# Kernel optimization log

Hardware: AMD Instinct MI355X
Metric: run time of the kernel (lower is better)

Reference implementation:

```python
import jax, jax.numpy as jnp
import numpy as np

N = 3072
E = 32 * N
H = 8
IN_F = 64
OUT_F = 16
ALPHA = 0.2  # LeakyReLU slope
NEG_INF = -9e15


def setup_inputs() -> dict:
    key = jax.random.key(0)
    k1, k2, k3, k4, k5 = jax.random.split(key, 5)
    h = jax.random.normal(k1, (N, IN_F), dtype=jnp.float32)
    edge_index = jax.random.randint(k2, (2, E), 0, N, dtype=jnp.int64)
    S = jax.random.uniform(k3, (N, N), dtype=jnp.float32)
    W = jax.random.normal(k4, (H, IN_F, OUT_F), dtype=jnp.float32) * 0.2
    a = jax.random.normal(k5, (H, 2 * OUT_F, 1), dtype=jnp.float32) * 0.3
    raw_gamma = jnp.ones((H,), dtype=jnp.float32)
    return {"h": h, "edge_index": edge_index, "S": S, "W": W, "a": a, "raw_gamma": raw_gamma}


def reference(h, edge_index, S, W, a, raw_gamma):
    n = h.shape[0]
    # dense adjacency from edge list (to_dense_adj semantics: adj[src, dst] += 1)
    adj = jnp.zeros((n, n), dtype=h.dtype).at[edge_index[0], edge_index[1]].add(1.0)
    # per-head projection: Wh [H, N, O]
    Wh = jnp.einsum('nf,hfo->hno', h, W)
    o = W.shape[2]
    a1 = a[:, :o, 0]  # [H, O]
    a2 = a[:, o:, 0]  # [H, O]
    e1 = jnp.einsum('hno,ho->hn', Wh, a1)  # Wh @ a[:O]
    e2 = jnp.einsum('hno,ho->hn', Wh, a2)  # Wh @ a[O:]
    e = jax.nn.leaky_relu(e1[:, :, None] + e2[:, None, :], ALPHA)  # [H, N, N]
    att = jnp.where(adj[None] > 0, e, jnp.asarray(NEG_INF, e.dtype))
    gamma = jax.nn.softplus(raw_gamma)  # [H], non-negative gate
    att = att * (1.0 + gamma[:, None, None] * S[None])
    att = jax.nn.softmax(att, axis=-1)  # row softmax (dim=1 of [N, N])
    # dropout is identity in eval mode
    h_prime = jnp.einsum('hnm,hmo->hno', att, Wh)  # [H, N, O]
    h_prime = jax.nn.elu(h_prime)  # concat=True per head
    # concat heads along feature dim -> [N, H*O]
    return jnp.transpose(h_prime, (1, 0, 2)).reshape(n, -1)
```

## Files before the change

kernel.cpp:

```cpp
#include <hip/hip_runtime.h>
#include <math.h>

#define N_NODES 3072
#define H_HEADS 8
#define IN_FEAT 64
#define OUT_FEAT 16
#define WORDS_PER_ROW (N_NODES / 32)
#define MAXD 1024

__global__ void zero_bits_kernel(unsigned int* __restrict__ bits, int n) {
    int i = blockIdx.x * blockDim.x + threadIdx.x;
    if (i < n) bits[i] = 0u;
}

__global__ void scatter_edges_kernel(const int* __restrict__ ei,
                                     unsigned int* __restrict__ bits, int E) {
    int e = blockIdx.x * blockDim.x + threadIdx.x;
    if (e >= E) return;
    int r = ei[e];
    int c = ei[E + e];
    atomicOr(&bits[r * WORDS_PER_ROW + (c >> 5)], 1u << (c & 31));
}

__global__ void compute_wh_kernel(const float* __restrict__ hfeat,
                                  const float* __restrict__ W,
                                  const float* __restrict__ a,
                                  float* __restrict__ Wh,
                                  float* __restrict__ e1,
                                  float* __restrict__ e2) {
    __shared__ float sh[IN_FEAT];
    int n = blockIdx.x;
    int tid = threadIdx.x;
    if (tid < IN_FEAT) sh[tid] = hfeat[n * IN_FEAT + tid];
    __syncthreads();
    int hh = tid >> 4, o = tid & 15;
    const float* wp = &W[hh * IN_FEAT * OUT_FEAT + o];
    float acc = 0.f;
#pragma unroll
    for (int f = 0; f < IN_FEAT; ++f) acc = fmaf(sh[f], wp[f * OUT_FEAT], acc);
    Wh[(hh * N_NODES + n) * OUT_FEAT + o] = acc;
    float p1 = acc * a[hh * 2 * OUT_FEAT + o];
    float p2 = acc * a[hh * 2 * OUT_FEAT + OUT_FEAT + o];
#pragma unroll
    for (int m = 1; m < 16; m <<= 1) {
        p1 += __shfl_xor(p1, m, 64);
        p2 += __shfl_xor(p2, m, 64);
    }
    if (o == 0) {
        e1[hh * N_NODES + n] = p1;
        e2[hh * N_NODES + n] = p2;
    }
}

__launch_bounds__(512)
__global__ void gat_main_kernel(const unsigned int* __restrict__ bits,
                                const float* __restrict__ S,
                                const float* __restrict__ Wh,
                                const float* __restrict__ e1,
                                const float* __restrict__ e2,
                                const float* __restrict__ raw_gamma,
                                float* __restrict__ out) {
    __shared__ int lds_j[MAXD];
    __shared__ float lds_s[MAXD];
    __shared__ int cnt_sh;
    __shared__ int fb_j;
    int i = blockIdx.x;
    int tid = threadIdx.x;
    if (tid == 0) cnt_sh = 0;
    __syncthreads();

    for (int w = tid; w < WORDS_PER_ROW; w += blockDim.x) {
        unsigned int b = bits[i * WORDS_PER_ROW + w];
        while (b) {
            int bit = __ffs(b) - 1;
            b &= b - 1;
            int j = w * 32 + bit;
            int pos = atomicAdd(&cnt_sh, 1);
            if (pos < MAXD) {
                lds_j[pos] = j;
                lds_s[pos] = S[i * N_NODES + j];
            }
        }
    }
    __syncthreads();
    int cnt = cnt_sh;
    if (cnt > MAXD) cnt = MAXD;

    int wave = tid >> 6, lane = tid & 63;
    int hh = wave;

    if (cnt == 0) {
        if (tid < 64) {
            float bm = 3.4e38f;
            int bj = 0;
            for (int j = tid; j < N_NODES; j += 64) {
                float s = S[i * N_NODES + j];
                if (s < bm) { bm = s; bj = j; }
            }
            for (int m = 1; m < 64; m <<= 1) {
                float bm2 = __shfl_xor(bm, m, 64);
                int bj2 = __shfl_xor(bj, m, 64);
                if (bm2 < bm || (bm2 == bm && bj2 < bj)) { bm = bm2; bj = bj2; }
            }
            if (tid == 0) fb_j = bj;
        }
        __syncthreads();
        int jj = fb_j;
        if (lane < OUT_FEAT) {
            float x = Wh[(hh * N_NODES + jj) * OUT_FEAT + lane];
            out[i * (H_HEADS * OUT_FEAT) + hh * OUT_FEAT + lane] =
                x > 0.f ? x : expm1f(x);
        }
        return;
    }

    float g = log1pf(expf(raw_gamma[hh]));
    float e1v = e1[hh * N_NODES + i];
    float m = -3.4e38f, l = 0.f;
    float acc[OUT_FEAT];
#pragma unroll
    for (int o = 0; o < OUT_FEAT; ++o) acc[o] = 0.f;

    for (int k = lane; k < cnt; k += 64) {
        int j = lds_j[k];
        float x = e1v + e2[hh * N_NODES + j];
        x = x > 0.f ? x : 0.2f * x;
        float v = x * (1.f + g * lds_s[k]);
        float mn = fmaxf(m, v);
        float sc = __expf(m - mn);
        float p = __expf(v - mn);
        l = l * sc + p;
        const float4* whp = (const float4*)&Wh[(hh * N_NODES + j) * OUT_FEAT];
        float4 w0 = whp[0], w1 = whp[1], w2 = whp[2], w3 = whp[3];
        acc[0] = acc[0] * sc + p * w0.x;  acc[1] = acc[1] * sc + p * w0.y;
        acc[2] = acc[2] * sc + p * w0.z;  acc[3] = acc[3] * sc + p * w0.w;
        acc[4] = acc[4] * sc + p * w1.x;  acc[5] = acc[5] * sc + p * w1.y;
        acc[6] = acc[6] * sc + p * w1.z;  acc[7] = acc[7] * sc + p * w1.w;
        acc[8] = acc[8] * sc + p * w2.x;  acc[9] = acc[9] * sc + p * w2.y;
        acc[10] = acc[10] * sc + p * w2.z; acc[11] = acc[11] * sc + p * w2.w;
        acc[12] = acc[12] * sc + p * w3.x; acc[13] = acc[13] * sc + p * w3.y;
        acc[14] = acc[14] * sc + p * w3.z; acc[15] = acc[15] * sc + p * w3.w;
        m = mn;
    }

    for (int msk = 1; msk < 64; msk <<= 1) {
        float m2 = __shfl_xor(m, msk, 64);
        float l2 = __shfl_xor(l, msk, 64);
        float mn = fmaxf(m, m2);
        float s1 = __expf(m - mn);
        float s2 = __expf(m2 - mn);
        l = l * s1 + l2 * s2;
#pragma unroll
        for (int o = 0; o < OUT_FEAT; ++o) {
            float av = __shfl_xor(acc[o], msk, 64);
            acc[o] = acc[o] * s1 + av * s2;
        }
        m = mn;
    }

    float inv = 1.f / l;
    float val = 0.f;
#pragma unroll
    for (int o = 0; o < OUT_FEAT; ++o)
        if (lane == o) val = acc[o];
    if (lane < OUT_FEAT) {
        float x = val * inv;
        out[i * (H_HEADS * OUT_FEAT) + hh * OUT_FEAT + lane] =
            x > 0.f ? x : expm1f(x);
    }
}

extern "C" void kernel_launch(void* const* d_in, const int* in_sizes, int n_in,
                              void* d_out, int out_size, void* d_ws, size_t ws_size,
                              hipStream_t stream) {
    const float* hfeat = (const float*)d_in[0];
    const int* ei      = (const int*)d_in[1];
    const float* S     = (const float*)d_in[2];
    const float* W     = (const float*)d_in[3];
    const float* a     = (const float*)d_in[4];
    const float* rg    = (const float*)d_in[5];
    float* out = (float*)d_out;

    char* ws = (char*)d_ws;
    unsigned int* bits = (unsigned int*)ws;
    float* Wh = (float*)(ws + 1179648);
    float* e1 = (float*)(ws + 1179648 + 1572864);
    float* e2 = e1 + H_HEADS * N_NODES;

    int nbits = N_NODES * WORDS_PER_ROW;
    zero_bits_kernel<<<(nbits + 255) / 256, 256, 0, stream>>>(bits, nbits);

    int E = in_sizes[1] / 2;
    scatter_edges_kernel<<<(E + 255) / 256, 256, 0, stream>>>(ei, bits, E);

    compute_wh_kernel<<<N_NODES, 128, 0, stream>>>(hfeat, W, a, Wh, e1, e2);

    gat_main_kernel<<<N_NODES, 512, 0, stream>>>(bits, S, Wh, e1, e2, rg, out);
}
```

Baseline: 128.8 us.

## Fuse edge scatter with Wh projection and restructure attention aggregation into two passes

Merges the edge-scatter and Wh/e1/e2 projection kernels into one launch that splits work by block index. The projection now stages W transposed in LDS and handles 16 nodes per block. The bitmask zeroing becomes hipMemsetAsync. In the main kernel, the online-softmax loop that carried 16 accumulators per lane is split in two: the first pass computes and stores scores in LDS while tracking max and sum, and the second pass spreads the weighted sum across lanes by output feature, which removes the 16-wide shuffle reduction. MAXD drops to 256, so rows with more than 256 neighbors would be truncated. The expected degree is about 32, so this is safe here but it is a tighter assumption.

```diff
diff --git a/kernel.cpp b/kernel.cpp
--- a/kernel.cpp
+++ b/kernel.cpp
@@ -6,49 +6,76 @@
 #define IN_FEAT 64
 #define OUT_FEAT 16
 #define WORDS_PER_ROW (N_NODES / 32)
-#define MAXD 1024
-
-__global__ void zero_bits_kernel(unsigned int* __restrict__ bits, int n) {
-    int i = blockIdx.x * blockDim.x + threadIdx.x;
-    if (i < n) bits[i] = 0u;
-}
-
-__global__ void scatter_edges_kernel(const int* __restrict__ ei,
-                                     unsigned int* __restrict__ bits, int E) {
-    int e = blockIdx.x * blockDim.x + threadIdx.x;
-    if (e >= E) return;
-    int r = ei[e];
-    int c = ei[E + e];
-    atomicOr(&bits[r * WORDS_PER_ROW + (c >> 5)], 1u << (c & 31));
-}
-
-__global__ void compute_wh_kernel(const float* __restrict__ hfeat,
-                                  const float* __restrict__ W,
-                                  const float* __restrict__ a,
-                                  float* __restrict__ Wh,
-                                  float* __restrict__ e1,
-                                  float* __restrict__ e2) {
-    __shared__ float sh[IN_FEAT];
-    int n = blockIdx.x;
+#define MAXD 256
+#define SCATTER_BLOCKS 384
+#define WH_NPB 16
+#define WH_BLOCKS (N_NODES / WH_NPB)
+
+__launch_bounds__(256)
+__global__ void scatter_and_wh_kernel(const int* __restrict__ ei, int E,
+                                      unsigned int* __restrict__ bits,
+                                      const float* __restrict__ hfeat,
+                                      const float* __restrict__ W,
+                                      const float* __restrict__ a,
+                                      float* __restrict__ Wh,
+                                      float* __restrict__ e1,
+                                      float* __restrict__ e2) {
+    __shared__ __align__(16) float Wt[H_HEADS][OUT_FEAT][68];
+    __shared__ __align__(16) float hs[WH_NPB][IN_FEAT];
+
     int tid = threadIdx.x;
-    if (tid < IN_FEAT) sh[tid] = hfeat[n * IN_FEAT + tid];
-    __syncthreads();
-    int hh = tid >> 4, o = tid & 15;
-    const float* wp = &W[hh * IN_FEAT * OUT_FEAT + o];
-    float acc = 0.f;
-#pragma unroll
-    for (int f = 0; f < IN_FEAT; ++f) acc = fmaf(sh[f], wp[f * OUT_FEAT], acc);
-    Wh[(hh * N_NODES + n) * OUT_FEAT + o] = acc;
-    float p1 = acc * a[hh * 2 * OUT_FEAT + o];
-    float p2 = acc * a[hh * 2 * OUT_FEAT + OUT_FEAT + o];
-#pragma unroll
-    for (int m = 1; m < 16; m <<= 1) {
-        p1 += __shfl_xor(p1, m, 64);
-        p2 += __shfl_xor(p2, m, 64);
-    }
-    if (o == 0) {
-        e1[hh * N_NODES + n] = p1;
-        e2[hh * N_NODES + n] = p2;
+    if (blockIdx.x < SCATTER_BLOCKS) {
+        int e = blockIdx.x * 256 + tid;
+        if (e < E) {
+            int r = ei[e];
+            int c = ei[E + e];
+            atomicOr(&bits[r * WORDS_PER_ROW + (c >> 5)], 1u << (c & 31));
+        }
+        return;
+    }
+
+    int node_base = (blockIdx.x - SCATTER_BLOCKS) * WH_NPB;
+    for (int idx = tid; idx < H_HEADS * IN_FEAT * OUT_FEAT; idx += 256) {
+        int hh = idx >> 10, f = (idx >> 4) & 63, o = idx & 15;
+        Wt[hh][o][f] = W[idx];
+    }
+    for (int idx = tid; idx < WH_NPB * IN_FEAT; idx += 256)
+        hs[idx >> 6][idx & 63] = hfeat[node_base * IN_FEAT + idx];
+    __syncthreads();
+
+    int ng = tid >> 7;
+    int hh = (tid >> 4) & 7;
+    int o  = tid & 15;
+    float a1v = a[hh * 2 * OUT_FEAT + o];
+    float a2v = a[hh * 2 * OUT_FEAT + OUT_FEAT + o];
+
+    float4 w[16];
+#pragma unroll
+    for (int q = 0; q < 16; ++q)
+        w[q] = *(const float4*)&Wt[hh][o][4 * q];
+
+    for (int n = ng; n < WH_NPB; n += 2) {
+        float acc = 0.f;
+#pragma unroll
+        for (int q = 0; q < 16; ++q) {
+            float4 hv = *(const float4*)&hs[n][4 * q];
+            acc = fmaf(hv.x, w[q].x, acc);
+            acc = fmaf(hv.y, w[q].y, acc);
+            acc = fmaf(hv.z, w[q].z, acc);
+            acc = fmaf(hv.w, w[q].w, acc);
+        }
+        int node = node_base + n;
+        Wh[(hh * N_NODES + node) * OUT_FEAT + o] = acc;
+        float p1 = acc * a1v, p2 = acc * a2v;
+#pragma unroll
+        for (int m = 1; m < 16; m <<= 1) {
+            p1 += __shfl_xor(p1, m, 64);
+            p2 += __shfl_xor(p2, m, 64);
+        }
+        if (o == 0) {
+            e1[hh * N_NODES + node] = p1;
+            e2[hh * N_NODES + node] = p2;
+        }
     }
 }
 
@@ -62,6 +89,7 @@
                                 float* __restrict__ out) {
     __shared__ int lds_j[MAXD];
     __shared__ float lds_s[MAXD];
+    __shared__ float lds_v[H_HEADS][MAXD];
     __shared__ int cnt_sh;
     __shared__ int fb_j;
     int i = blockIdx.x;
@@ -86,8 +114,8 @@
     int cnt = cnt_sh;
     if (cnt > MAXD) cnt = MAXD;
 
-    int wave = tid >> 6, lane = tid & 63;
-    int hh = wave;
+    int lane = tid & 63;
+    int hh = tid >> 6;
 
     if (cnt == 0) {
         if (tid < 64) {
@@ -117,55 +145,37 @@
     float g = log1pf(expf(raw_gamma[hh]));
     float e1v = e1[hh * N_NODES + i];
     float m = -3.4e38f, l = 0.f;
-    float acc[OUT_FEAT];
-#pragma unroll
-    for (int o = 0; o < OUT_FEAT; ++o) acc[o] = 0.f;
-
     for (int k = lane; k < cnt; k += 64) {
         int j = lds_j[k];
         float x = e1v + e2[hh * N_NODES + j];
         x = x > 0.f ? x : 0.2f * x;
         float v = x * (1.f + g * lds_s[k]);
+        lds_v[hh][k] = v;
         float mn = fmaxf(m, v);
-        float sc = __expf(m - mn);
-        float p = __expf(v - mn);
-        l = l * sc + p;
-        const float4* whp = (const float4*)&Wh[(hh * N_NODES + j) * OUT_FEAT];
-        float4 w0 = whp[0], w1 = whp[1], w2 = whp[2], w3 = whp[3];
-        acc[0] = acc[0] * sc + p * w0.x;  acc[1] = acc[1] * sc + p * w0.y;
-        acc[2] = acc[2] * sc + p * w0.z;  acc[3] = acc[3] * sc + p * w0.w;
-        acc[4] = acc[4] * sc + p * w1.x;  acc[5] = acc[5] * sc + p * w1.y;
-        acc[6] = acc[6] * sc + p * w1.z;  acc[7] = acc[7] * sc + p * w1.w;
-        acc[8] = acc[8] * sc + p * w2.x;  acc[9] = acc[9] * sc + p * w2.y;
-        acc[10] = acc[10] * sc + p * w2.z; acc[11] = acc[11] * sc + p * w2.w;
-        acc[12] = acc[12] * sc + p * w3.x; acc[13] = acc[13] * sc + p * w3.y;
-        acc[14] = acc[14] * sc + p * w3.z; acc[15] = acc[15] * sc + p * w3.w;
+        l = l * __expf(m - mn) + __expf(v - mn);
         m = mn;
     }
-
+#pragma unroll
     for (int msk = 1; msk < 64; msk <<= 1) {
         float m2 = __shfl_xor(m, msk, 64);
         float l2 = __shfl_xor(l, msk, 64);
         float mn = fmaxf(m, m2);
-        float s1 = __expf(m - mn);
-        float s2 = __expf(m2 - mn);
-        l = l * s1 + l2 * s2;
-#pragma unroll
-        for (int o = 0; o < OUT_FEAT; ++o) {
-            float av = __shfl_xor(acc[o], msk, 64);
-            acc[o] = acc[o] * s1 + av * s2;
-        }
+        l = l * __expf(m - mn) + l2 * __expf(m2 - mn);
         m = mn;
     }
-
-    float inv = 1.f / l;
-    float val = 0.f;
-#pragma unroll
-    for (int o = 0; o < OUT_FEAT; ++o)
-        if (lane == o) val = acc[o];
-    if (lane < OUT_FEAT) {
-        float x = val * inv;
-        out[i * (H_HEADS * OUT_FEAT) + hh * OUT_FEAT + lane] =
+    __syncthreads();
+
+    int kgrp = lane >> 4, o = lane & 15;
+    float acc = 0.f;
+    for (int kk = kgrp; kk < cnt; kk += 4) {
+        float p = __expf(lds_v[hh][kk] - m);
+        acc = fmaf(p, Wh[(hh * N_NODES + lds_j[kk]) * OUT_FEAT + o], acc);
+    }
+    acc += __shfl_xor(acc, 16, 64);
+    acc += __shfl_xor(acc, 32, 64);
+    if (kgrp == 0) {
+        float x = acc / l;
+        out[i * (H_HEADS * OUT_FEAT) + hh * OUT_FEAT + o] =
             x > 0.f ? x : expm1f(x);
     }
 }
@@ -188,12 +198,11 @@
     float* e2 = e1 + H_HEADS * N_NODES;
 
     int nbits = N_NODES * WORDS_PER_ROW;
-    zero_bits_kernel<<<(nbits + 255) / 256, 256, 0, stream>>>(bits, nbits);
+    hipMemsetAsync(bits, 0, (size_t)nbits * 4, stream);
 
     int E = in_sizes[1] / 2;
-    scatter_edges_kernel<<<(E + 255) / 256, 256, 0, stream>>>(ei, bits, E);
-
-    compute_wh_kernel<<<N_NODES, 128, 0, stream>>>(hfeat, W, a, Wh, e1, e2);
+    scatter_and_wh_kernel<<<SCATTER_BLOCKS + WH_BLOCKS, 256, 0, stream>>>(
+        ei, E, bits, hfeat, W, a, Wh, e1, e2);
 
     gat_main_kernel<<<N_NODES, 512, 0, stream>>>(bits, S, Wh, e1, e2, rg, out);
 }
```

Measured after the change: 117.6 us. -8.7%, faster.
